# Optimization experiments

Measured on AMD Instinct MI355X. Metric: run time of the kernel, lower is better.

Reference implementation:

```python
import jax, jax.numpy as jnp
import numpy as np

APERTURE = 256
IGNORE_ITSELF = False
FMAX = jnp.float32(3.4028235e38)  # tf.float32.max


def setup_inputs() -> dict:
    key = jax.random.key(0)
    ks = jax.random.split(key, 5)
    n, m, d = 4096, 1024, 1024
    scale = 1.0 / np.sqrt(m)
    x = jax.random.normal(ks[0], (n, m), dtype=jnp.float32)
    WK = jax.random.normal(ks[1], (m, d), dtype=jnp.float32) * scale
    WQ = jax.random.normal(ks[2], (m, d), dtype=jnp.float32) * scale
    WV = jax.random.normal(ks[3], (m, d), dtype=jnp.float32) * scale
    Wout = jax.random.normal(ks[4], (d, m), dtype=jnp.float32) * scale
    return {"x": x, "WK": WK, "WQ": WQ, "WV": WV, "Wout": Wout}


def reference(x, WK, WQ, WV, Wout):
    n = x.shape[0]
    K = x @ WK                      # [n, d]
    Q = (x @ WQ) * 0.06             # [n, d]
    V = x @ WV                      # [n, d]
    logits = Q @ K.T                # [n, n]

    i = jnp.arange(n)[:, None]
    j = jnp.arange(n)[None, :]
    if IGNORE_ITSELF:
        keep = (i != j).astype(jnp.float32)
        logits = logits * keep - FMAX * (1.0 - keep)
    if APERTURE > 0:
        # tf: mask = 1 - band_part(ones, -aperture, aperture); negative num_lower
        # keeps the whole lower triangle, so mask==1 exactly where j - i > aperture.
        keep = (j - i > APERTURE).astype(jnp.float32)
        logits = logits * keep - FMAX * (1.0 - keep)

    att_weights = jax.nn.softmax(logits, axis=-1)  # [n, n]
    # dropout is identity (training=False). NOTE faithful quirk: transpose_a=True.
    y = att_weights.T @ V           # [n, d]
    y = y @ Wout                    # [n, m]
    return (y, att_weights)
```

## Files before the change

kernel.cpp:

```cpp
#include <hip/hip_runtime.h>
#include <cstdint>
#include <cstddef>

#define N_TOK 4096
#define M_DIM 1024
#define APER  256
constexpr float FMAXV = 3.4028235e38f;

typedef __attribute__((ext_vector_type(8))) short short8;
typedef __attribute__((ext_vector_type(4))) float float4_t;

__device__ __forceinline__ unsigned short f2bf(float x) {
    union { float f; uint32_t u; } v; v.f = x;
    uint32_t u = v.u;
    u += 0x7FFFu + ((u >> 16) & 1u);
    return (unsigned short)(u >> 16);
}

__device__ __forceinline__ void gload16(const void* g, void* l) {
    __builtin_amdgcn_global_load_lds(
        (const __attribute__((address_space(1))) void*)g,
        (__attribute__((address_space(3))) void*)l, 16, 0, 0);
}

__global__ __launch_bounds__(256) void cast_bf16(const float* __restrict__ src,
                                                 unsigned short* __restrict__ dst, int n) {
    const int i = (blockIdx.x * 256 + threadIdx.x) * 4;
    if (i >= n) return;
    const float4 v = *reinterpret_cast<const float4*>(&src[i]);
    ushort4 o;
    o.x = f2bf(v.x); o.y = f2bf(v.y); o.z = f2bf(v.z); o.w = f2bf(v.w);
    *reinterpret_cast<ushort4*>(&dst[i]) = o;
}

__global__ __launch_bounds__(256) void wtrans3(const float* __restrict__ W0, const float* __restrict__ W1,
                                               const float* __restrict__ W2,
                                               unsigned short* __restrict__ D0, unsigned short* __restrict__ D1,
                                               unsigned short* __restrict__ D2) {
    const int z = blockIdx.z;
    const float* src = z == 0 ? W0 : (z == 1 ? W1 : W2);
    unsigned short* dst = z == 0 ? D0 : (z == 1 ? D1 : D2);
    __shared__ unsigned short tile[32][33];
    const int c0 = blockIdx.x * 32, r0 = blockIdx.y * 32;
    const int tx = threadIdx.x & 31, ty = threadIdx.x >> 5;
#pragma unroll
    for (int i = ty; i < 32; i += 8)
        tile[i][tx] = f2bf(src[(size_t)(r0 + i) * M_DIM + c0 + tx]);
    __syncthreads();
#pragma unroll
    for (int i = ty; i < 32; i += 8)
        dst[(size_t)(c0 + i) * M_DIM + r0 + tx] = tile[tx][i];
}

__global__ __launch_bounds__(256) void transpose_bf16(const unsigned short* __restrict__ src,
                                                      unsigned short* __restrict__ dst,
                                                      int R, int C) {
    __shared__ unsigned short tile[32][33];
    const int c0 = blockIdx.x * 32, r0 = blockIdx.y * 32;
    const int tx = threadIdx.x & 31, ty = threadIdx.x >> 5;
#pragma unroll
    for (int i = ty; i < 32; i += 8)
        tile[i][tx] = src[(size_t)(r0 + i) * C + c0 + tx];
    __syncthreads();
#pragma unroll
    for (int i = ty; i < 32; i += 8)
        dst[(size_t)(c0 + i) * R + r0 + tx] = tile[tx][i];
}

template <int SKIP>
__global__ __launch_bounds__(256) void nt64sq(const unsigned short* __restrict__ A,
                                              const unsigned short* __restrict__ B,
                                              float* __restrict__ Cf,
                                              unsigned short* __restrict__ Cb,
                                              int N, int K, float alpha) {
    const int by   = (SKIP == 1) ? ((int)gridDim.y - 1 - (int)blockIdx.y) : (int)blockIdx.y;
    const int row0 = by * 64;
    const int col0 = blockIdx.x * 64;

    __shared__ unsigned short Asb[64 * 32];
    __shared__ unsigned short Bsb[64 * 32];

    const int t = threadIdx.x, w = t >> 6, lane = t & 63;
    float4_t acc[4] = {};

    const int sr   = lane >> 2;
    const int sk   = ((lane & 3) ^ ((sr >> 1) & 3)) * 8;
    const int m    = lane & 15;
    const int slot = ((lane >> 4) ^ ((m >> 1) & 3)) * 8;

    for (int k0 = 0; k0 < K; k0 += 32) {
        if (SKIP == 1) {
            if ((k0 > row0 + 63 - APER - 1) && (k0 + 31 < N_TOK - APER - 1)) continue;
        }
        const int rr = w * 16 + sr;
        gload16(&A[(size_t)(row0 + rr) * K + k0 + sk], &Asb[w * 512]);
        gload16(&B[(size_t)(col0 + rr) * K + k0 + sk], &Bsb[w * 512]);
        __syncthreads();
        const short8 af = *reinterpret_cast<const short8*>(&Asb[(w * 16 + m) * 32 + slot]);
        short8 bf[4];
#pragma unroll
        for (int j = 0; j < 4; ++j)
            bf[j] = *reinterpret_cast<const short8*>(&Bsb[(j * 16 + m) * 32 + slot]);
#pragma unroll
        for (int j = 0; j < 4; ++j)
            acc[j] = __builtin_amdgcn_mfma_f32_16x16x32_bf16(af, bf[j], acc[j], 0, 0, 0);
        __syncthreads();
    }

    const int crow = row0 + w * 16 + (lane >> 4) * 4;
    const int ccol = col0 + m;
#pragma unroll
    for (int j = 0; j < 4; ++j)
#pragma unroll
        for (int r = 0; r < 4; ++r) {
            const float v = alpha * acc[j][r];
            const size_t idx = (size_t)(crow + r) * N + ccol + j * 16;
            if (Cf) Cf[idx] = v;
            if (Cb) Cb[idx] = f2bf(v);
        }
}

__global__ __launch_bounds__(256) void mfma_qkv(const unsigned short* __restrict__ xb,
                                                const unsigned short* __restrict__ WKt,
                                                const unsigned short* __restrict__ WQt,
                                                const unsigned short* __restrict__ WVWt,
                                                unsigned short* __restrict__ Kb,
                                                unsigned short* __restrict__ Qb,
                                                unsigned short* __restrict__ VWb) {
    const int row0  = blockIdx.y * 128;
    const int col0g = blockIdx.x * 128;
    const int seg   = col0g >> 10;
    const int col0  = col0g & 1023;
    const unsigned short* B = seg == 0 ? WKt : (seg == 1 ? WQt : WVWt);
    unsigned short*       C = seg == 0 ? Kb  : (seg == 1 ? Qb  : VWb);
    const float alpha = (seg == 1) ? 0.06f : 1.0f;

    __shared__ unsigned short Asb[128 * 32];
    __shared__ unsigned short Bsb[128 * 32];

    const int t = threadIdx.x, w = t >> 6, lane = t & 63;
    const int wr = (w >> 1) * 64, wc = (w & 1) * 64;

    float4_t acc[4][4] = {};

    const int sr   = lane >> 2;
    const int sk   = ((lane & 3) ^ ((sr >> 1) & 3)) * 8;
    const int m    = lane & 15;
    const int slot = ((lane >> 4) ^ ((m >> 1) & 3)) * 8;

    for (int k0 = 0; k0 < M_DIM; k0 += 32) {
#pragma unroll
        for (int cc = 0; cc < 2; ++cc) {
            const int c = 2 * w + cc;
            const int rr = c * 16 + sr;
            gload16(&xb[(size_t)(row0 + rr) * M_DIM + k0 + sk], &Asb[c * 512]);
            gload16(&B[(size_t)(col0 + rr) * M_DIM + k0 + sk], &Bsb[c * 512]);
        }
        __syncthreads();
        short8 af[4], bf[4];
#pragma unroll
        for (int i = 0; i < 4; ++i)
            af[i] = *reinterpret_cast<const short8*>(&Asb[(wr + i * 16 + m) * 32 + slot]);
#pragma unroll
        for (int j = 0; j < 4; ++j)
            bf[j] = *reinterpret_cast<const short8*>(&Bsb[(wc + j * 16 + m) * 32 + slot]);
#pragma unroll
        for (int i = 0; i < 4; ++i)
#pragma unroll
            for (int j = 0; j < 4; ++j)
                acc[i][j] = __builtin_amdgcn_mfma_f32_16x16x32_bf16(af[i], bf[j], acc[i][j], 0, 0, 0);
        __syncthreads();
    }

    const int crow = row0 + wr + (lane >> 4) * 4;
    const int ccol = col0 + wc + m;
#pragma unroll
    for (int i = 0; i < 4; ++i)
#pragma unroll
        for (int j = 0; j < 4; ++j)
#pragma unroll
            for (int r = 0; r < 4; ++r)
                C[(size_t)(crow + i * 16 + r) * M_DIM + ccol + j * 16] = f2bf(alpha * acc[i][j][r]);
}

__global__ __launch_bounds__(256) void mfma_logits_exp(const unsigned short* __restrict__ A,
                                                       const unsigned short* __restrict__ B,
                                                       float* __restrict__ att,
                                                       float* __restrict__ rowsum) {
    const int row0 = blockIdx.y * 128;
    const int col0 = blockIdx.x * 128;
    if (col0 + 127 <= row0 + APER) return;

    __shared__ unsigned short Asb[128 * 32];
    __shared__ unsigned short Bsb[128 * 32];

    const int t = threadIdx.x, w = t >> 6, lane = t & 63;
    const int wr = (w >> 1) * 64, wc = (w & 1) * 64;

    float4_t acc[4][4] = {};

    const int sr   = lane >> 2;
    const int sk   = ((lane & 3) ^ ((sr >> 1) & 3)) * 8;
    const int m    = lane & 15;
    const int slot = ((lane >> 4) ^ ((m >> 1) & 3)) * 8;

    for (int k0 = 0; k0 < M_DIM; k0 += 32) {
#pragma unroll
        for (int cc = 0; cc < 2; ++cc) {
            const int c = 2 * w + cc;
            const int rr = c * 16 + sr;
            gload16(&A[(size_t)(row0 + rr) * M_DIM + k0 + sk], &Asb[c * 512]);
            gload16(&B[(size_t)(col0 + rr) * M_DIM + k0 + sk], &Bsb[c * 512]);
        }
        __syncthreads();
        short8 af[4], bf[4];
#pragma unroll
        for (int i = 0; i < 4; ++i)
            af[i] = *reinterpret_cast<const short8*>(&Asb[(wr + i * 16 + m) * 32 + slot]);
#pragma unroll
        for (int j = 0; j < 4; ++j)
            bf[j] = *reinterpret_cast<const short8*>(&Bsb[(wc + j * 16 + m) * 32 + slot]);
#pragma unroll
        for (int i = 0; i < 4; ++i)
#pragma unroll
            for (int j = 0; j < 4; ++j)
                acc[i][j] = __builtin_amdgcn_mfma_f32_16x16x32_bf16(af[i], bf[j], acc[i][j], 0, 0, 0);
        __syncthreads();
    }

    const int crow = row0 + wr + (lane >> 4) * 4;
    const int ccol = col0 + wc + m;
#pragma unroll
    for (int i = 0; i < 4; ++i) {
#pragma unroll
        for (int r = 0; r < 4; ++r) {
            const int gr = crow + i * 16 + r;
            float partial = 0.0f;
#pragma unroll
            for (int j = 0; j < 4; ++j) {
                const int gc = ccol + j * 16;
                const float e = __expf(acc[i][j][r]);
                att[(size_t)gr * N_TOK + gc] = e;
                if (gc > gr + APER) partial += e;
            }
            partial += __shfl_xor(partial, 1, 64);
            partial += __shfl_xor(partial, 2, 64);
            partial += __shfl_xor(partial, 4, 64);
            partial += __shfl_xor(partial, 8, 64);
            if (m == 0) atomicAdd(&rowsum[gr], partial);
        }
    }
}

__global__ __launch_bounds__(256) void zero_rowsum(float* __restrict__ rowsum) {
    const int i = (blockIdx.x * 256 + threadIdx.x) * 4;
    float4 z; z.x = z.y = z.z = z.w = 0.0f;
    *reinterpret_cast<float4*>(&rowsum[i]) = z;
}

__global__ __launch_bounds__(256) void normalize_att(float* __restrict__ att,
                                                     const float* __restrict__ rowsum) {
    const int i = blockIdx.x;
    const int t = threadIdx.x;
    float4* row4 = reinterpret_cast<float4*>(att + (size_t)i * N_TOK);
    const int jstart = i + APER + 1;

    if (jstart >= N_TOK) {
        const float u = 1.0f / (float)N_TOK;
        float4 uv; uv.x = uv.y = uv.z = uv.w = u;
        for (int q = t; q < N_TOK / 4; q += 256) row4[q] = uv;
        return;
    }

    const float inv = 1.0f / rowsum[i];
    const int q0 = jstart >> 2;
    float4 z; z.x = z.y = z.z = z.w = 0.0f;
    for (int q = t; q < q0; q += 256) row4[q] = z;
    for (int q = q0 + t; q < N_TOK / 4; q += 256) {
        float4 v = row4[q];
        const int j = q * 4;
        v.x = (j + 0 >= jstart) ? v.x * inv : 0.0f;
        v.y = (j + 1 >= jstart) ? v.y * inv : 0.0f;
        v.z = (j + 2 >= jstart) ? v.z * inv : 0.0f;
        v.w = v.w * inv;
        row4[q] = v;
    }
}

__global__ __launch_bounds__(256) void att_transpose(const float* __restrict__ src,
                                                     unsigned short* __restrict__ dst) {
    const int c0 = blockIdx.x * 32, r0 = blockIdx.y * 32;
    const int t = threadIdx.x;
    if ((c0 + 31 <= r0 + APER) && (r0 + 31 < N_TOK - APER - 1)) {
        const int rr = t >> 3;
        const int cc = (t & 7) * 4;
        ushort4 z; z.x = z.y = z.z = z.w = 0;
        *reinterpret_cast<ushort4*>(&dst[(size_t)(c0 + rr) * N_TOK + r0 + cc]) = z;
        return;
    }
    __shared__ unsigned short tile[32][33];
    const int tx = t & 31, ty = t >> 5;
#pragma unroll
    for (int i = ty; i < 32; i += 8)
        tile[i][tx] = f2bf(src[(size_t)(r0 + i) * N_TOK + c0 + tx]);
    __syncthreads();
#pragma unroll
    for (int i = ty; i < 32; i += 8)
        dst[(size_t)(c0 + i) * N_TOK + r0 + tx] = tile[tx][i];
}

extern "C" void kernel_launch(void* const* d_in, const int* in_sizes, int n_in,
                              void* d_out, int out_size, void* d_ws, size_t ws_size,
                              hipStream_t stream) {
    const float* x    = (const float*)d_in[0];
    const float* WK   = (const float*)d_in[1];
    const float* WQ   = (const float*)d_in[2];
    const float* WV   = (const float*)d_in[3];
    const float* Wout = (const float*)d_in[4];

    float* y   = (float*)d_out;
    float* att = y + (size_t)N_TOK * M_DIM;

    unsigned short* base = (unsigned short*)d_ws;
    const size_t MEG = 1u << 20;
    unsigned short* xb    = base;
    unsigned short* WKt   = base + 4  * MEG;
    unsigned short* WQt   = base + 5  * MEG;
    unsigned short* Woutt = base + 6  * MEG;
    unsigned short* WVb   = base + 7  * MEG;
    unsigned short* WVWt  = base + 8  * MEG;
    unsigned short* Kb    = base + 9  * MEG;
    unsigned short* Qb    = base + 13 * MEG;
    unsigned short* VWb   = base + 17 * MEG;
    unsigned short* attT  = base + 4  * MEG;
    float*          rowsum = (float*)(base + 20 * MEG);
    unsigned short* VWt   = xb;

    const dim3 blk(256);

    cast_bf16<<<dim3((N_TOK * M_DIM) / 1024), blk, 0, stream>>>(x, xb, N_TOK * M_DIM);
    cast_bf16<<<dim3((M_DIM * M_DIM) / 1024), blk, 0, stream>>>(WV, WVb, M_DIM * M_DIM);
    wtrans3<<<dim3(M_DIM / 32, M_DIM / 32, 3), blk, 0, stream>>>(WK, WQ, Wout, WKt, WQt, Woutt);

    nt64sq<0><<<dim3(M_DIM / 64, M_DIM / 64), blk, 0, stream>>>(Woutt, WVb, nullptr, WVWt,
                                                                M_DIM, M_DIM, 1.0f);

    mfma_qkv<<<dim3(24, N_TOK / 128), blk, 0, stream>>>(xb, WKt, WQt, WVWt, Kb, Qb, VWb);

    transpose_bf16<<<dim3(M_DIM / 32, N_TOK / 32), blk, 0, stream>>>(VWb, VWt, N_TOK, M_DIM);

    zero_rowsum<<<dim3(4), blk, 0, stream>>>(rowsum);
    mfma_logits_exp<<<dim3(N_TOK / 128, N_TOK / 128), blk, 0, stream>>>(Qb, Kb, att, rowsum);

    normalize_att<<<dim3(N_TOK), blk, 0, stream>>>(att, rowsum);

    att_transpose<<<dim3(N_TOK / 32, N_TOK / 32), blk, 0, stream>>>(att, attT);

    nt64sq<1><<<dim3(M_DIM / 64, N_TOK / 64), blk, 0, stream>>>(attT, VWt, y, nullptr,
                                                                M_DIM, N_TOK, 1.0f);
}
```

Baseline: 296.6 us.

## Fuse attention normalization with bf16 transpose and mask inside logits epilogue

Merges the row-normalize and transpose-to-bf16 kernels into one tiled finalize kernel that reads each attention element once, scales it, writes the fp32 result and the transposed bf16 copy. The logits epilogue now applies the band mask directly, writing zeros for masked entries and ones for fully-masked rows, and initializes those rows' sums to N so normalization yields uniform weights. This cuts a full read/write pass over the 64MB attention matrix and one launch, and skips exp on masked entries, at the cost of a larger finalize tile with shared-memory transposition.

Measured after the change: 290.1 us. 2.2% less time.

```diff
diff --git a/kernel.cpp b/kernel.cpp
--- a/kernel.cpp
+++ b/kernel.cpp
@@ -5,7 +5,7 @@
 #define N_TOK 4096
 #define M_DIM 1024
 #define APER  256
-constexpr float FMAXV = 3.4028235e38f;
+#define UNIF_START 3839
 
 typedef __attribute__((ext_vector_type(8))) short short8;
 typedef __attribute__((ext_vector_type(4))) float float4_t;
@@ -72,7 +72,7 @@
                                               const unsigned short* __restrict__ B,
                                               float* __restrict__ Cf,
                                               unsigned short* __restrict__ Cb,
-                                              int N, int K, float alpha) {
+                                              int N, int K) {
     const int by   = (SKIP == 1) ? ((int)gridDim.y - 1 - (int)blockIdx.y) : (int)blockIdx.y;
     const int row0 = by * 64;
     const int col0 = blockIdx.x * 64;
@@ -90,7 +90,7 @@
 
     for (int k0 = 0; k0 < K; k0 += 32) {
         if (SKIP == 1) {
-            if ((k0 > row0 + 63 - APER - 1) && (k0 + 31 < N_TOK - APER - 1)) continue;
+            if ((k0 > row0 + 63 - APER - 1) && (k0 + 31 < UNIF_START)) continue;
         }
         const int rr = w * 16 + sr;
         gload16(&A[(size_t)(row0 + rr) * K + k0 + sk], &Asb[w * 512]);
@@ -113,7 +113,7 @@
     for (int j = 0; j < 4; ++j)
 #pragma unroll
         for (int r = 0; r < 4; ++r) {
-            const float v = alpha * acc[j][r];
+            const float v = acc[j][r];
             const size_t idx = (size_t)(crow + r) * N + ccol + j * 16;
             if (Cf) Cf[idx] = v;
             if (Cb) Cb[idx] = f2bf(v);
@@ -239,74 +239,86 @@
 #pragma unroll
             for (int j = 0; j < 4; ++j) {
                 const int gc = ccol + j * 16;
-                const float e = __expf(acc[i][j][r]);
-                att[(size_t)gr * N_TOK + gc] = e;
-                if (gc > gr + APER) partial += e;
+                float val;
+                if (gr >= UNIF_START) {
+                    val = 1.0f;
+                } else if (gc > gr + APER) {
+                    val = __expf(acc[i][j][r]);
+                    partial += val;
+                } else {
+                    val = 0.0f;
+                }
+                att[(size_t)gr * N_TOK + gc] = val;
             }
             partial += __shfl_xor(partial, 1, 64);
             partial += __shfl_xor(partial, 2, 64);
             partial += __shfl_xor(partial, 4, 64);
             partial += __shfl_xor(partial, 8, 64);
-            if (m == 0) atomicAdd(&rowsum[gr], partial);
-        }
-    }
-}
-
-__global__ __launch_bounds__(256) void zero_rowsum(float* __restrict__ rowsum) {
-    const int i = (blockIdx.x * 256 + threadIdx.x) * 4;
-    float4 z; z.x = z.y = z.z = z.w = 0.0f;
-    *reinterpret_cast<float4*>(&rowsum[i]) = z;
-}
-
-__global__ __launch_bounds__(256) void normalize_att(float* __restrict__ att,
-                                                     const float* __restrict__ rowsum) {
-    const int i = blockIdx.x;
+            if (m == 0 && gr < UNIF_START) atomicAdd(&rowsum[gr], partial);
+        }
+    }
+}
+
+__global__ __launch_bounds__(256) void init_rowsum(float* __restrict__ rowsum) {
+    const int i = blockIdx.x * 256 + threadIdx.x;
+    if (i < N_TOK) rowsum[i] = (i >= UNIF_START) ? (float)N_TOK : 0.0f;
+}
+
+__global__ __launch_bounds__(256) void finalize_att(float* __restrict__ att,
+                                                    unsigned short* __restrict__ attT,
+                                                    const float* __restrict__ rowsum) {
+    const int j0 = blockIdx.x * 64, i0 = blockIdx.y * 64;
     const int t = threadIdx.x;
-    float4* row4 = reinterpret_cast<float4*>(att + (size_t)i * N_TOK);
-    const int jstart = i + APER + 1;
-
-    if (jstart >= N_TOK) {
-        const float u = 1.0f / (float)N_TOK;
-        float4 uv; uv.x = uv.y = uv.z = uv.w = u;
-        for (int q = t; q < N_TOK / 4; q += 256) row4[q] = uv;
+    const int rl = t >> 4;
+    const int c4 = (t & 15) * 4;
+    const float u = 1.0f / (float)N_TOK;
+
+    if (j0 + 63 <= i0 + APER) {
+#pragma unroll
+        for (int s = 0; s < 4; ++s) {
+            const int i = i0 + rl + 16 * s;
+            const float val = (i >= UNIF_START) ? u : 0.0f;
+            float4 v; v.x = v.y = v.z = v.w = val;
+            *reinterpret_cast<float4*>(&att[(size_t)i * N_TOK + j0 + c4]) = v;
+        }
+        const unsigned short bu = f2bf(u);
+#pragma unroll
+        for (int s = 0; s < 4; ++s) {
+            const int j = j0 + rl + 16 * s;
+            ushort4 o;
+            o.x = (i0 + c4 + 0 >= UNIF_START) ? bu : 0;
+            o.y = (i0 + c4 + 1 >= UNIF_START) ? bu : 0;
+            o.z = (i0 + c4 + 2 >= UNIF_START) ? bu : 0;
+            o.w = (i0 + c4 + 3 >= UNIF_START) ? bu : 0;
+            *reinterpret_cast<ushort4*>(&attT[(size_t)j * N_TOK + i0 + c4]) = o;
+        }
         return;
     }
 
-    const float inv = 1.0f / rowsum[i];
-    const int q0 = jstart >> 2;
-    float4 z; z.x = z.y = z.z = z.w = 0.0f;
-    for (int q = t; q < q0; q += 256) row4[q] = z;
-    for (int q = q0 + t; q < N_TOK / 4; q += 256) {
-        float4 v = row4[q];
-        const int j = q * 4;
-        v.x = (j + 0 >= jstart) ? v.x * inv : 0.0f;
-        v.y = (j + 1 >= jstart) ? v.y * inv : 0.0f;
-        v.z = (j + 2 >= jstart) ? v.z * inv : 0.0f;
-        v.w = v.w * inv;
-        row4[q] = v;
-    }
-}
-
-__global__ __launch_bounds__(256) void att_transpose(const float* __restrict__ src,
-                                                     unsigned short* __restrict__ dst) {
-    const int c0 = blockIdx.x * 32, r0 = blockIdx.y * 32;
-    const int t = threadIdx.x;
-    if ((c0 + 31 <= r0 + APER) && (r0 + 31 < N_TOK - APER - 1)) {
-        const int rr = t >> 3;
-        const int cc = (t & 7) * 4;
-        ushort4 z; z.x = z.y = z.z = z.w = 0;
-        *reinterpret_cast<ushort4*>(&dst[(size_t)(c0 + rr) * N_TOK + r0 + cc]) = z;
-        return;
-    }
-    __shared__ unsigned short tile[32][33];
-    const int tx = t & 31, ty = t >> 5;
-#pragma unroll
-    for (int i = ty; i < 32; i += 8)
-        tile[i][tx] = f2bf(src[(size_t)(r0 + i) * N_TOK + c0 + tx]);
+    __shared__ unsigned short tile[64][72];
+#pragma unroll
+    for (int s = 0; s < 4; ++s) {
+        const int il = rl + 16 * s;
+        const int i  = i0 + il;
+        const float inv = 1.0f / rowsum[i];
+        float4 v = *reinterpret_cast<const float4*>(&att[(size_t)i * N_TOK + j0 + c4]);
+        v.x *= inv; v.y *= inv; v.z *= inv; v.w *= inv;
+        *reinterpret_cast<float4*>(&att[(size_t)i * N_TOK + j0 + c4]) = v;
+        ushort4 b;
+        b.x = f2bf(v.x); b.y = f2bf(v.y); b.z = f2bf(v.z); b.w = f2bf(v.w);
+        *reinterpret_cast<ushort4*>(&tile[il][c4]) = b;
+    }
     __syncthreads();
 #pragma unroll
-    for (int i = ty; i < 32; i += 8)
-        dst[(size_t)(c0 + i) * N_TOK + r0 + tx] = tile[tx][i];
+    for (int s = 0; s < 4; ++s) {
+        const int jl = rl + 16 * s;
+        ushort4 o;
+        o.x = tile[c4 + 0][jl];
+        o.y = tile[c4 + 1][jl];
+        o.z = tile[c4 + 2][jl];
+        o.w = tile[c4 + 3][jl];
+        *reinterpret_cast<ushort4*>(&attT[(size_t)(j0 + jl) * N_TOK + i0 + c4]) = o;
+    }
 }
 
 extern "C" void kernel_launch(void* const* d_in, const int* in_sizes, int n_in,
@@ -343,19 +355,17 @@
     wtrans3<<<dim3(M_DIM / 32, M_DIM / 32, 3), blk, 0, stream>>>(WK, WQ, Wout, WKt, WQt, Woutt);
 
     nt64sq<0><<<dim3(M_DIM / 64, M_DIM / 64), blk, 0, stream>>>(Woutt, WVb, nullptr, WVWt,
-                                                                M_DIM, M_DIM, 1.0f);
+                                                                M_DIM, M_DIM);
 
     mfma_qkv<<<dim3(24, N_TOK / 128), blk, 0, stream>>>(xb, WKt, WQt, WVWt, Kb, Qb, VWb);
 
     transpose_bf16<<<dim3(M_DIM / 32, N_TOK / 32), blk, 0, stream>>>(VWb, VWt, N_TOK, M_DIM);
 
-    zero_rowsum<<<dim3(4), blk, 0, stream>>>(rowsum);
+    init_rowsum<<<dim3(N_TOK / 256), blk, 0, stream>>>(rowsum);
     mfma_logits_exp<<<dim3(N_TOK / 128, N_TOK / 128), blk, 0, stream>>>(Qb, Kb, att, rowsum);
 
-    normalize_att<<<dim3(N_TOK), blk, 0, stream>>>(att, rowsum);
-
-    att_transpose<<<dim3(N_TOK / 32, N_TOK / 32), blk, 0, stream>>>(att, attT);
+    finalize_att<<<dim3(N_TOK / 64, N_TOK / 64), blk, 0, stream>>>(att, attT, rowsum);
 
     nt64sq<1><<<dim3(M_DIM / 64, N_TOK / 64), blk, 0, stream>>>(attT, VWt, y, nullptr,
-                                                                M_DIM, N_TOK, 1.0f);
-}
+                                                                M_DIM, N_TOK);
+}
```
